# Kernel optimization log

Hardware: AMD Instinct MI355X
Metric: run time of the kernel (lower is better)

## Reference

```python
import jax, jax.numpy as jnp
import numpy as np

B, S, D, N_OPS = 16, 8192, 128, 4


def setup_inputs() -> dict:
    key = jax.random.key(0)
    k1, k2, k3 = jax.random.split(key, 3)
    x = jax.random.normal(k1, (B, S, D), dtype=jnp.float32)
    # candidate op parameters: 4 Linear(D, D) layers, stacked
    W = jax.random.normal(k2, (N_OPS, D, D), dtype=jnp.float32) * (1.0 / np.sqrt(D))
    b = jax.random.normal(k3, (N_OPS, D), dtype=jnp.float32) * 0.01
    # one-hot path selector buffer: weights[0] = 1.0 (as in MixModule.__init__)
    weights = jnp.zeros((N_OPS,), dtype=jnp.float32).at[0].set(1.0)
    return {"x": x, "W": W, "b": b, "weights": weights}


def reference(x, W, b, weights):
    # Faithful to the torch loop: compute EVERY candidate op(x), then the
    # weighted (one-hot) sum. outs: [B, S, n_ops, D]
    outs = jnp.einsum("bsd,ofd->bsof", x, W) + b[None, None, :, :]
    y = jnp.einsum("bsof,o->bsf", outs, weights)
    return y
```

## Files before the change

### kernel.cpp

```cpp
#include <hip/hip_runtime.h>
#include <hip/hip_bf16.h>

#define D 128
#define NOPS 4
#define BS_STRIDE 136

typedef __attribute__((ext_vector_type(8))) short short8;
typedef __attribute__((ext_vector_type(4))) float float4_t;

__global__ void combine_kernel(const float* __restrict__ W,
                               const float* __restrict__ b,
                               const float* __restrict__ wts,
                               __hip_bfloat16* __restrict__ Wc,
                               float* __restrict__ bc) {
    int idx = blockIdx.x * blockDim.x + threadIdx.x;
    float w0 = wts[0], w1 = wts[1], w2 = wts[2], w3 = wts[3];
    if (idx < D * D) {
        float v = w0 * W[idx] + w1 * W[D * D + idx]
                + w2 * W[2 * D * D + idx] + w3 * W[3 * D * D + idx];
        Wc[idx] = __float2bfloat16(v);
    }
    if (idx < D) {
        bc[idx] = w0 * b[idx] + w1 * b[D + idx] + w2 * b[2 * D + idx] + w3 * b[3 * D + idx];
    }
}

__device__ inline short8 cvt8_bf16(float4_t a, float4_t b) {
    union { short8 s; __hip_bfloat16 h[8]; } u;
    u.h[0] = __float2bfloat16(a[0]);
    u.h[1] = __float2bfloat16(a[1]);
    u.h[2] = __float2bfloat16(a[2]);
    u.h[3] = __float2bfloat16(a[3]);
    u.h[4] = __float2bfloat16(b[0]);
    u.h[5] = __float2bfloat16(b[1]);
    u.h[6] = __float2bfloat16(b[2]);
    u.h[7] = __float2bfloat16(b[3]);
    return u.s;
}

__global__ __launch_bounds__(256) void gemm_kernel(const float* __restrict__ x,
                                                   const __hip_bfloat16* __restrict__ Wc,
                                                   const float* __restrict__ bc,
                                                   float* __restrict__ y,
                                                   int M) {
    __shared__ __align__(16) __hip_bfloat16 Bs[D * BS_STRIDE];

    const int tid  = threadIdx.x;
    const int lane = tid & 63;
    const int wave = tid >> 6;

    #pragma unroll
    for (int i = 0; i < 8; i++) {
        int c  = i * 256 + tid;
        int n  = c >> 4;
        int ko = (c & 15) << 3;
        short8 v = *(const short8*)((const short*)Wc + n * D + ko);
        *(short8*)((short*)Bs + n * BS_STRIDE + ko) = v;
    }
    __syncthreads();

    const int m0 = (blockIdx.x * 4 + wave) * 16;
    if (m0 >= M) return;

    const int row  = lane & 15;
    const int quad = lane >> 4;

    float4_t acc[8];
    #pragma unroll
    for (int i = 0; i < 8; i++) acc[i] = (float4_t)(0.f);

    #pragma unroll
    for (int ks = 0; ks < 4; ks++) {
        const float* ap = x + (size_t)(m0 + row) * D + ks * 32 + quad * 8;
        float4_t a0 = *(const float4_t*)ap;
        float4_t a1 = *(const float4_t*)(ap + 4);
        short8 afrag = cvt8_bf16(a0, a1);

        const short* bp = (const short*)Bs + ks * 32 + quad * 8;
        #pragma unroll
        for (int nt = 0; nt < 8; nt++) {
            short8 bfrag = *(const short8*)(bp + (nt * 16 + row) * BS_STRIDE);
            acc[nt] = __builtin_amdgcn_mfma_f32_16x16x32_bf16(afrag, bfrag, acc[nt], 0, 0, 0);
        }
    }

    #pragma unroll
    for (int nt = 0; nt < 8; nt++) {
        int col = nt * 16 + row;
        float bias = bc[col];
        #pragma unroll
        for (int r = 0; r < 4; r++) {
            int m = m0 + quad * 4 + r;
            y[(size_t)m * D + col] = acc[nt][r] + bias;
        }
    }
}

extern "C" void kernel_launch(void* const* d_in, const int* in_sizes, int n_in,
                              void* d_out, int out_size, void* d_ws, size_t ws_size,
                              hipStream_t stream) {
    const float* x   = (const float*)d_in[0];
    const float* W   = (const float*)d_in[1];
    const float* b   = (const float*)d_in[2];
    const float* wts = (const float*)d_in[3];
    float* y = (float*)d_out;

    __hip_bfloat16* Wc = (__hip_bfloat16*)d_ws;
    float* bc = (float*)((char*)d_ws + D * D * sizeof(__hip_bfloat16));

    combine_kernel<<<(D * D + 255) / 256, 256, 0, stream>>>(W, b, wts, Wc, bc);

    const int M = in_sizes[0] / D;
    gemm_kernel<<<M / 64, 256, 0, stream>>>(x, Wc, bc, y, M);
}
```

Before: 123.3 us.

## Transpose MFMA operands for vectorized stores and double rows per wave

Swaps the MFMA operand roles so the weight fragment from LDS is the A operand and x rows are the B operand, which puts each lane's accumulator on four consecutive output columns and allows 16-byte float4 stores of y and vector bias loads. Each wave now computes 32 rows instead of 16, reusing every LDS weight fragment across two MFMAs and halving the grid. The launch bounds also request 4 blocks per SM. This roughly doubles accumulator registers and reduces the number of blocks that share the cost of staging weights into LDS.

```diff
diff --git a/kernel.cpp b/kernel.cpp
--- a/kernel.cpp
+++ b/kernel.cpp
@@ -2,7 +2,6 @@
 #include <hip/hip_bf16.h>
 
 #define D 128
-#define NOPS 4
 #define BS_STRIDE 136
 
 typedef __attribute__((ext_vector_type(8))) short short8;
@@ -38,11 +37,11 @@
     return u.s;
 }
 
-__global__ __launch_bounds__(256) void gemm_kernel(const float* __restrict__ x,
-                                                   const __hip_bfloat16* __restrict__ Wc,
-                                                   const float* __restrict__ bc,
-                                                   float* __restrict__ y,
-                                                   int M) {
+__global__ __launch_bounds__(256, 4) void gemm_kernel(const float* __restrict__ x,
+                                                      const __hip_bfloat16* __restrict__ Wc,
+                                                      const float* __restrict__ bc,
+                                                      float* __restrict__ y,
+                                                      int M) {
     __shared__ __align__(16) __hip_bfloat16 Bs[D * BS_STRIDE];
 
     const int tid  = threadIdx.x;
@@ -59,39 +58,43 @@
     }
     __syncthreads();
 
-    const int m0 = (blockIdx.x * 4 + wave) * 16;
-    if (m0 >= M) return;
+    const int l15  = lane & 15;
+    const int quad = lane >> 4;
+    const int m_base = blockIdx.x * 128 + wave * 32;
+    if (m_base >= M) return;
 
-    const int row  = lane & 15;
-    const int quad = lane >> 4;
+    float4_t acc[2][8];
+    #pragma unroll
+    for (int t = 0; t < 2; t++)
+        #pragma unroll
+        for (int nt = 0; nt < 8; nt++) acc[t][nt] = (float4_t)(0.f);
 
-    float4_t acc[8];
-    #pragma unroll
-    for (int i = 0; i < 8; i++) acc[i] = (float4_t)(0.f);
+    const float* xr0 = x + (size_t)(m_base + l15) * D;
+    const float* xr1 = xr0 + 16 * D;
 
     #pragma unroll
     for (int ks = 0; ks < 4; ks++) {
-        const float* ap = x + (size_t)(m0 + row) * D + ks * 32 + quad * 8;
-        float4_t a0 = *(const float4_t*)ap;
-        float4_t a1 = *(const float4_t*)(ap + 4);
-        short8 afrag = cvt8_bf16(a0, a1);
-
-        const short* bp = (const short*)Bs + ks * 32 + quad * 8;
+        const int koff = ks * 32 + quad * 8;
+        short8 b0 = cvt8_bf16(*(const float4_t*)(xr0 + koff),
+                              *(const float4_t*)(xr0 + koff + 4));
+        short8 b1 = cvt8_bf16(*(const float4_t*)(xr1 + koff),
+                              *(const float4_t*)(xr1 + koff + 4));
+        const short* ap = (const short*)Bs + koff;
         #pragma unroll
         for (int nt = 0; nt < 8; nt++) {
-            short8 bfrag = *(const short8*)(bp + (nt * 16 + row) * BS_STRIDE);
-            acc[nt] = __builtin_amdgcn_mfma_f32_16x16x32_bf16(afrag, bfrag, acc[nt], 0, 0, 0);
+            short8 af = *(const short8*)(ap + (nt * 16 + l15) * BS_STRIDE);
+            acc[0][nt] = __builtin_amdgcn_mfma_f32_16x16x32_bf16(af, b0, acc[0][nt], 0, 0, 0);
+            acc[1][nt] = __builtin_amdgcn_mfma_f32_16x16x32_bf16(af, b1, acc[1][nt], 0, 0, 0);
         }
     }
 
     #pragma unroll
     for (int nt = 0; nt < 8; nt++) {
-        int col = nt * 16 + row;
-        float bias = bc[col];
+        float4_t bias = *(const float4_t*)(bc + nt * 16 + quad * 4);
         #pragma unroll
-        for (int r = 0; r < 4; r++) {
-            int m = m0 + quad * 4 + r;
-            y[(size_t)m * D + col] = acc[nt][r] + bias;
+        for (int t = 0; t < 2; t++) {
+            float4_t v = acc[t][nt] + bias;
+            *(float4_t*)(y + (size_t)(m_base + t * 16 + l15) * D + nt * 16 + quad * 4) = v;
         }
     }
 }
@@ -111,5 +114,5 @@
     combine_kernel<<<(D * D + 255) / 256, 256, 0, stream>>>(W, b, wts, Wc, bc);
 
     const int M = in_sizes[0] / D;
-    gemm_kernel<<<M / 64, 256, 0, stream>>>(x, Wc, bc, y, M);
+    gemm_kernel<<<M / 128, 256, 0, stream>>>(x, Wc, bc, y, M);
 }
```

Result: slower. 126.0 us (+2.2%).
